# Performance work log

Hardware: AMD Instinct MI355X
Metric: run time of the kernel (lower is better)

## Reference

```python
import jax, jax.numpy as jnp
import numpy as np

# PyG ChebConv defaults: normalization='sym', lambda_max=2.0.
# L_hat = 2*L/lambda_max - I = (I - D^-1/2 A D^-1/2) - I = -D^-1/2 A D^-1/2
# (self-loop/diagonal coefficient is exactly 0 when lambda_max == 2).

N_NODES = 30000
IN_CH = 128
HID_CH = 256
K = 3
N_EDGES = 480000


def _norm_weights(edge_index, n):
    src, dst = edge_index[0], edge_index[1]
    mask = src != dst  # remove_self_loops
    ones = jnp.where(mask, 1.0, 0.0)
    deg = jax.ops.segment_sum(ones, src, num_segments=n)
    dis = jnp.where(deg > 0, deg ** -0.5, 0.0)  # deg_inv_sqrt, inf -> 0
    w = jnp.where(mask, -dis[src] * dis[dst], 0.0)  # -A_sym edge weights
    return src, dst, w


def _cheb_conv(x, src, dst, w, W, b, n):
    # Tx_0 = x; Tx_1 = L_hat x; Tx_k = 2 L_hat Tx_{k-1} - Tx_{k-2}
    def lap(h):  # sparse matvec: (L_hat h)[i] = sum_{e: dst_e=i} w_e * h[src_e]
        return jax.ops.segment_sum(w[:, None] * h[src], dst, num_segments=n)

    Tx_prev = x
    out = x @ W[0]
    if W.shape[0] > 1:
        Tx_cur = lap(x)
        out = out + Tx_cur @ W[1]
        for k in range(2, W.shape[0]):
            Tx_next = 2.0 * lap(Tx_cur) - Tx_prev
            out = out + Tx_next @ W[k]
            Tx_prev, Tx_cur = Tx_cur, Tx_next
    return out + b


def setup_inputs() -> dict:
    key = jax.random.key(0)
    k1, k2, k3, k4, k5, k6 = jax.random.split(key, 6)
    x = jax.random.normal(k1, (N_NODES, IN_CH), dtype=jnp.float32)
    edge_index = jax.random.randint(k2, (2, N_EDGES), 0, N_NODES, dtype=jnp.int64)
    s1 = (1.0 / (IN_CH * K)) ** 0.5
    s2 = (1.0 / (HID_CH * K)) ** 0.5
    W1 = jax.random.uniform(k3, (K, IN_CH, HID_CH), jnp.float32, -s1, s1)
    b1 = jax.random.uniform(k4, (HID_CH,), jnp.float32, -s1, s1)
    W2 = jax.random.uniform(k5, (K, HID_CH, IN_CH), jnp.float32, -s2, s2)
    b2 = jax.random.uniform(k6, (IN_CH,), jnp.float32, -s2, s2)
    return {"x": x, "edge_index": edge_index, "W1": W1, "b1": b1, "W2": W2, "b2": b2}


def reference(x, edge_index, W1, b1, W2, b2):
    n = x.shape[0]
    src, dst, w = _norm_weights(edge_index, n)
    h = jax.nn.relu(_cheb_conv(x, src, dst, w, W1, b1, n))
    return _cheb_conv(h, src, dst, w, W2, b2, n)
```

## Files before the change

### kernel.cpp

```cpp
#include <hip/hip_runtime.h>
#include <hip/hip_bf16.h>


#define ELLW 64

typedef short bf16x8_t __attribute__((ext_vector_type(8)));
typedef unsigned short u16x4_t __attribute__((ext_vector_type(4)));
typedef unsigned short u16x8_t __attribute__((ext_vector_type(8)));
typedef float f32x4_t __attribute__((ext_vector_type(4)));

static __device__ inline unsigned short f2bf(float f) {
    __hip_bfloat16 h = __float2bfloat16(f);
    return __builtin_bit_cast(unsigned short, h);
}
static __device__ inline float bfbits2f(unsigned int lo16) {
    unsigned int u = lo16 << 16;
    return __builtin_bit_cast(float, u);
}

__global__ __launch_bounds__(256) void build_kernel(const int* __restrict__ src,
                                                    const int* __restrict__ dst,
                                                    int* __restrict__ degi,
                                                    int* __restrict__ cnt,
                                                    int* __restrict__ ell, int E) {
    int e = blockIdx.x * 256 + threadIdx.x;
    if (e >= E) return;
    int s = src[e], d = dst[e];
    if (s != d) atomicAdd(&degi[s], 1);
    int pos = atomicAdd(&cnt[d], 1);
    if (pos < ELLW) ell[(size_t)d * ELLW + pos] = s;
}

__global__ __launch_bounds__(256) void dis_kernel(const int* __restrict__ degi,
                                                  float* __restrict__ dis, int N) {
    int i = blockIdx.x * 256 + threadIdx.x;
    if (i >= N) return;
    int d = degi[i];
    dis[i] = (d > 0) ? rsqrtf((float)d) : 0.0f;
}

__global__ __launch_bounds__(256) void bt1_kernel(const float* __restrict__ W1,
                                                  unsigned short* __restrict__ Bt1) {
    int i = blockIdx.x * 256 + threadIdx.x;
    if (i >= 256 * 384) return;
    int n = i / 384, k = i % 384;
    Bt1[(size_t)n * 384 + k] = f2bf(W1[(size_t)k * 256 + n]);
}

__global__ __launch_bounds__(256) void bt2_kernel(const float* __restrict__ W2,
                                                  unsigned short* __restrict__ Bt2) {
    int i = blockIdx.x * 256 + threadIdx.x;
    if (i >= 384 * 256) return;
    int n = i / 256, k = i % 256;
    float v;
    if (n < 128) v = W2[(size_t)(1 * 256 + k) * 128 + n];
    else if (n < 256) v = W2[(size_t)(2 * 256 + k) * 128 + (n - 128)];
    else v = W2[(size_t)k * 128 + (n - 256)] - W2[(size_t)(2 * 256 + k) * 128 + (n - 256)];
    Bt2[(size_t)n * 256 + k] = f2bf(v);
}

__global__ __launch_bounds__(256) void f2bf_kernel(const float* __restrict__ X,
                                                   unsigned short* __restrict__ Xb, int n4) {
    int i = blockIdx.x * 256 + threadIdx.x;
    if (i >= n4) return;
    f32x4_t v = *(const f32x4_t*)&X[(size_t)i * 4];
    u16x4_t u;
    u.x = f2bf(v.x); u.y = f2bf(v.y); u.z = f2bf(v.z); u.w = f2bf(v.w);
    *(u16x4_t*)&Xb[(size_t)i * 4] = u;
}

__global__ __launch_bounds__(256) void lap_ell_kernel(const unsigned short* __restrict__ Xb,
                                                      float* __restrict__ Yf,
                                                      unsigned short* __restrict__ Yb,
                                                      const int* __restrict__ cnt,
                                                      const int* __restrict__ ell,
                                                      const float* __restrict__ dis,
                                                      const float* __restrict__ add,
                                                      const float* __restrict__ bias,
                                                      float s, float a, int N) {
    int wave = threadIdx.x >> 6;
    int lane = threadIdx.x & 63;
    int node = blockIdx.x * 4 + wave;
    if (node >= N) return;
    int n = cnt[node];
    if (n > ELLW) n = ELLW;
    float disn = dis[node];
    const int* row = ell + (size_t)node * ELLW;

    float ax0 = 0.f, ay0 = 0.f, ax1 = 0.f, ay1 = 0.f;
    float ax2 = 0.f, ay2 = 0.f, ax3 = 0.f, ay3 = 0.f;
    int j = 0;
    for (; j + 4 <= n; j += 4) {
        int4 s4 = *(const int4*)&row[j];
        int s0 = __builtin_amdgcn_readfirstlane(s4.x);
        int s1 = __builtin_amdgcn_readfirstlane(s4.y);
        int s2 = __builtin_amdgcn_readfirstlane(s4.z);
        int s3 = __builtin_amdgcn_readfirstlane(s4.w);
        unsigned int v0 = *(const unsigned int*)&Xb[(size_t)s0 * 128 + lane * 2];
        unsigned int v1 = *(const unsigned int*)&Xb[(size_t)s1 * 128 + lane * 2];
        unsigned int v2 = *(const unsigned int*)&Xb[(size_t)s2 * 128 + lane * 2];
        unsigned int v3 = *(const unsigned int*)&Xb[(size_t)s3 * 128 + lane * 2];
        float w0 = (s0 != node) ? -disn * dis[s0] : 0.0f;
        float w1 = (s1 != node) ? -disn * dis[s1] : 0.0f;
        float w2 = (s2 != node) ? -disn * dis[s2] : 0.0f;
        float w3 = (s3 != node) ? -disn * dis[s3] : 0.0f;
        ax0 = fmaf(w0, bfbits2f(v0 & 0xffffu), ax0);
        ay0 = fmaf(w0, bfbits2f(v0 >> 16), ay0);
        ax1 = fmaf(w1, bfbits2f(v1 & 0xffffu), ax1);
        ay1 = fmaf(w1, bfbits2f(v1 >> 16), ay1);
        ax2 = fmaf(w2, bfbits2f(v2 & 0xffffu), ax2);
        ay2 = fmaf(w2, bfbits2f(v2 >> 16), ay2);
        ax3 = fmaf(w3, bfbits2f(v3 & 0xffffu), ax3);
        ay3 = fmaf(w3, bfbits2f(v3 >> 16), ay3);
    }
    for (; j < n; ++j) {
        int s0 = __builtin_amdgcn_readfirstlane(row[j]);
        unsigned int v0 = *(const unsigned int*)&Xb[(size_t)s0 * 128 + lane * 2];
        float w0 = (s0 != node) ? -disn * dis[s0] : 0.0f;
        ax0 = fmaf(w0, bfbits2f(v0 & 0xffffu), ax0);
        ay0 = fmaf(w0, bfbits2f(v0 >> 16), ay0);
    }
    float rx = s * ((ax0 + ax1) + (ax2 + ax3));
    float ry = s * ((ay0 + ay1) + (ay2 + ay3));
    size_t o = (size_t)node * 128 + lane * 2;
    if (add) {
        float2 ad = *(const float2*)&add[o];
        rx = fmaf(a, ad.x, rx);
        ry = fmaf(a, ad.y, ry);
    }
    if (bias) {
        rx += bias[lane * 2];
        ry += bias[lane * 2 + 1];
    }
    if (Yf) {
        float2 r; r.x = rx; r.y = ry;
        *(float2*)&Yf[o] = r;
    }
    if (Yb) {
        unsigned int ob = ((unsigned int)f2bf(ry) << 16) | f2bf(rx);
        *(unsigned int*)&Yb[o] = ob;
    }
}

__global__ __launch_bounds__(256) void gemm_mfma_kernel(
        const unsigned short* __restrict__ A0, const unsigned short* __restrict__ A1,
        const unsigned short* __restrict__ A2, int ldA,
        const unsigned short* __restrict__ Bt, int K,
        float* __restrict__ Of0, float* __restrict__ Of1, float* __restrict__ Of2,
        unsigned short* __restrict__ Ob0, unsigned short* __restrict__ Ob1,
        unsigned short* __restrict__ Ob2,
        int ldO, const float* __restrict__ bias, int M, int relu) {
    __shared__ unsigned short As[64][72];
    __shared__ unsigned short Bs[64][72];

    int tid = threadIdx.x;
    int lane = tid & 63;
    int wid = tid >> 6;
    int wm = wid >> 1, wn = wid & 1;
    int lm = lane & 15, lg = lane >> 4;

    int rowBase = blockIdx.x * 64;
    int colBase = blockIdx.y * 64;

    f32x4_t acc[2][2] = {};

    for (int k0 = 0; k0 < K; k0 += 64) {
        int seg = k0 >> 7;
        int acol = k0 & 127;
        const unsigned short* A = (seg == 0) ? A0 : ((seg == 1) ? A1 : A2);

        {
            int row = tid >> 2;
            int c = (tid & 3) * 16;
            int gr = rowBase + row;
            u16x8_t v0 = {0, 0, 0, 0, 0, 0, 0, 0};
            u16x8_t v1 = {0, 0, 0, 0, 0, 0, 0, 0};
            if (gr < M) {
                const unsigned short* ap = &A[(size_t)gr * ldA + acol + c];
                v0 = *(const u16x8_t*)ap;
                v1 = *(const u16x8_t*)(ap + 8);
            }
            *(u16x8_t*)&As[row][c] = v0;
            *(u16x8_t*)&As[row][c + 8] = v1;
        }
#pragma unroll
        for (int it = 0; it < 2; ++it) {
            int f = tid + it * 256;
            int n = f >> 3;
            int kb = f & 7;
            u16x8_t bv = *(const u16x8_t*)&Bt[(size_t)(colBase + n) * K + k0 + kb * 8];
            *(u16x8_t*)&Bs[n][kb * 8] = bv;
        }
        __syncthreads();

#pragma unroll
        for (int ks = 0; ks < 2; ++ks) {
            int koff = ks * 32 + lg * 8;
            bf16x8_t a0 = *(const bf16x8_t*)&As[wm * 32 + lm][koff];
            bf16x8_t a1 = *(const bf16x8_t*)&As[wm * 32 + 16 + lm][koff];
            bf16x8_t b0 = *(const bf16x8_t*)&Bs[wn * 32 + lm][koff];
            bf16x8_t b1 = *(const bf16x8_t*)&Bs[wn * 32 + 16 + lm][koff];
            acc[0][0] = __builtin_amdgcn_mfma_f32_16x16x32_bf16(a0, b0, acc[0][0], 0, 0, 0);
            acc[0][1] = __builtin_amdgcn_mfma_f32_16x16x32_bf16(a0, b1, acc[0][1], 0, 0, 0);
            acc[1][0] = __builtin_amdgcn_mfma_f32_16x16x32_bf16(a1, b0, acc[1][0], 0, 0, 0);
            acc[1][1] = __builtin_amdgcn_mfma_f32_16x16x32_bf16(a1, b1, acc[1][1], 0, 0, 0);
        }
        __syncthreads();
    }

    int oseg = colBase >> 7;
    float* Of = (oseg == 0) ? Of0 : ((oseg == 1) ? Of1 : Of2);
    unsigned short* Ob = (oseg == 0) ? Ob0 : ((oseg == 1) ? Ob1 : Ob2);
    int lcbase = (colBase & 127) + wn * 32;
#pragma unroll
    for (int i = 0; i < 2; ++i) {
#pragma unroll
        for (int j = 0; j < 2; ++j) {
            int lc = lcbase + j * 16 + lm;
            int gcol = colBase + wn * 32 + j * 16 + lm;
            float bval = bias ? bias[gcol] : 0.0f;
#pragma unroll
            for (int r = 0; r < 4; ++r) {
                int gr = rowBase + wm * 32 + i * 16 + lg * 4 + r;
                if (gr < M) {
                    float v = acc[i][j][r] + bval;
                    if (relu) v = fmaxf(v, 0.0f);
                    if (Of) Of[(size_t)gr * ldO + lc] = v;
                    if (Ob) Ob[(size_t)gr * ldO + lc] = f2bf(v);
                }
            }
        }
    }
}

extern "C" void kernel_launch(void* const* d_in, const int* in_sizes, int n_in,
                              void* d_out, int out_size, void* d_ws, size_t ws_size,
                              hipStream_t stream) {
    const float* x  = (const float*)d_in[0];
    const int*   ei = (const int*)d_in[1];
    const float* W1 = (const float*)d_in[2];
    const float* b1 = (const float*)d_in[3];
    const float* W2 = (const float*)d_in[4];
    const float* b2 = (const float*)d_in[5];
    float* out = (float*)d_out;

    const int IN = 128, HID = 256;
    int N = in_sizes[0] / IN;
    int E = in_sizes[1] / 2;
    const int* src = ei;
    const int* dst = ei + E;

    char* ws = (char*)d_ws;
    size_t off = 0;
    auto alloc = [&](size_t bytes) -> void* {
        void* p = ws + off;
        off += (bytes + 255) & ~(size_t)255;
        return p;
    };
    int* ibuf   = (int*)alloc((size_t)2 * N * 4);
    int* degi   = ibuf;
    int* cnt    = ibuf + N;
    float* dis  = (float*)alloc((size_t)N * 4);
    int* ell    = (int*)alloc((size_t)N * ELLW * 4);
    unsigned short* xb  = (unsigned short*)alloc((size_t)N * IN * 2);
    unsigned short* T1b = (unsigned short*)alloc((size_t)N * IN * 2);
    unsigned short* T2b = (unsigned short*)alloc((size_t)N * IN * 2);
    unsigned short* A2b = (unsigned short*)alloc((size_t)N * IN * 2);
    unsigned short* Ib  = (unsigned short*)alloc((size_t)N * IN * 2);
    unsigned short* hb  = (unsigned short*)alloc((size_t)N * HID * 2);
    float* D    = (float*)alloc((size_t)N * IN * 4);
    float* Z    = (float*)alloc((size_t)N * IN * 4);
    unsigned short* Bt1 = (unsigned short*)alloc((size_t)256 * 384 * 2);
    unsigned short* Bt2 = (unsigned short*)alloc((size_t)384 * 256 * 2);

    int gE = (E + 255) / 256;
    int gN = (N + 255) / 256;
    int gLap = (N + 3) / 4;
    int gBlkM = (N + 63) / 64;

    hipMemsetAsync(ibuf, 0, (size_t)2 * N * 4, stream);
    build_kernel<<<gE, 256, 0, stream>>>(src, dst, degi, cnt, ell, E);
    dis_kernel<<<gN, 256, 0, stream>>>(degi, dis, N);
    bt1_kernel<<<(256 * 384 + 255) / 256, 256, 0, stream>>>(W1, Bt1);
    bt2_kernel<<<(384 * 256 + 255) / 256, 256, 0, stream>>>(W2, Bt2);
    f2bf_kernel<<<(N * IN / 4 + 255) / 256, 256, 0, stream>>>(x, xb, N * IN / 4);

    lap_ell_kernel<<<gLap, 256, 0, stream>>>(xb, nullptr, T1b, cnt, ell, dis,
                                             nullptr, nullptr, 1.0f, 0.0f, N);
    lap_ell_kernel<<<gLap, 256, 0, stream>>>(T1b, nullptr, T2b, cnt, ell, dis,
                                             x, nullptr, 2.0f, -1.0f, N);
    {
        dim3 grid(gBlkM, 4);
        gemm_mfma_kernel<<<grid, 256, 0, stream>>>(xb, T1b, T2b, IN,
                                                   Bt1, 384,
                                                   nullptr, nullptr, nullptr,
                                                   hb, hb + 128, nullptr,
                                                   HID, b1, N, 1);
    }

    {
        dim3 grid(gBlkM, 6);
        gemm_mfma_kernel<<<grid, 256, 0, stream>>>(hb, hb + 128, nullptr, HID,
                                                   Bt2, 256,
                                                   D, nullptr, Z,
                                                   nullptr, A2b, nullptr,
                                                   IN, nullptr, N, 0);
        lap_ell_kernel<<<gLap, 256, 0, stream>>>(A2b, nullptr, Ib, cnt, ell, dis,
                                                 D, nullptr, 2.0f, 1.0f, N);
        lap_ell_kernel<<<gLap, 256, 0, stream>>>(Ib, out, nullptr, cnt, ell, dis,
                                                 Z, b2, 1.0f, 1.0f, N);
    }
}
```

Measured before the change: 220.6 us.

## Fuse prep kernels, drop dis buffer, store GEMM outputs in bf16, enlarge GEMM tile

Merges the weight-transpose and x-to-bf16 conversion kernels into a single prep kernel and removes dis_kernel; edge weights are now computed in the Laplacian kernel via rsqrt of the degree product. The build kernel handles two edges per thread. GEMM intermediates D and Z and the residual x are stored and read as bf16 instead of fp32, which cuts memory traffic at some cost in precision. The GEMM block becomes 512 threads covering 128 rows. It is unclear whether the A-tile loading code (not shown) was updated to fill 128 rows, and the wave-to-tile mapping may not cover the enlarged tile.

```diff
diff --git a/kernel.cpp b/kernel.cpp
--- a/kernel.cpp
+++ b/kernel.cpp
@@ -23,50 +23,54 @@
                                                     int* __restrict__ degi,
                                                     int* __restrict__ cnt,
                                                     int* __restrict__ ell, int E) {
-    int e = blockIdx.x * 256 + threadIdx.x;
-    if (e >= E) return;
-    int s = src[e], d = dst[e];
-    if (s != d) atomicAdd(&degi[s], 1);
-    int pos = atomicAdd(&cnt[d], 1);
-    if (pos < ELLW) ell[(size_t)d * ELLW + pos] = s;
-}
-
-__global__ __launch_bounds__(256) void dis_kernel(const int* __restrict__ degi,
-                                                  float* __restrict__ dis, int N) {
+    int base = (blockIdx.x * 256 + threadIdx.x) * 2;
+    if (base >= E) return;
+    if (base + 2 <= E) {
+        int2 s2 = *(const int2*)&src[base];
+        int2 d2 = *(const int2*)&dst[base];
+        if (s2.x != d2.x) atomicAdd(&degi[s2.x], 1);
+        if (s2.y != d2.y) atomicAdd(&degi[s2.y], 1);
+        int p0 = atomicAdd(&cnt[d2.x], 1);
+        int p1 = atomicAdd(&cnt[d2.y], 1);
+        if (p0 < ELLW) ell[(size_t)d2.x * ELLW + p0] = s2.x;
+        if (p1 < ELLW) ell[(size_t)d2.y * ELLW + p1] = s2.y;
+    } else {
+        int s = src[base], d = dst[base];
+        if (s != d) atomicAdd(&degi[s], 1);
+        int p = atomicAdd(&cnt[d], 1);
+        if (p < ELLW) ell[(size_t)d * ELLW + p] = s;
+    }
+}
+
+__global__ __launch_bounds__(256) void prep_kernel(const float* __restrict__ W1,
+                                                   const float* __restrict__ W2,
+                                                   const float* __restrict__ x,
+                                                   unsigned short* __restrict__ Bt1,
+                                                   unsigned short* __restrict__ Bt2,
+                                                   unsigned short* __restrict__ xb,
+                                                   int nx4) {
+    const int NB1 = 256 * 384, NB2 = 384 * 256;
     int i = blockIdx.x * 256 + threadIdx.x;
-    if (i >= N) return;
-    int d = degi[i];
-    dis[i] = (d > 0) ? rsqrtf((float)d) : 0.0f;
-}
-
-__global__ __launch_bounds__(256) void bt1_kernel(const float* __restrict__ W1,
-                                                  unsigned short* __restrict__ Bt1) {
-    int i = blockIdx.x * 256 + threadIdx.x;
-    if (i >= 256 * 384) return;
-    int n = i / 384, k = i % 384;
-    Bt1[(size_t)n * 384 + k] = f2bf(W1[(size_t)k * 256 + n]);
-}
-
-__global__ __launch_bounds__(256) void bt2_kernel(const float* __restrict__ W2,
-                                                  unsigned short* __restrict__ Bt2) {
-    int i = blockIdx.x * 256 + threadIdx.x;
-    if (i >= 384 * 256) return;
-    int n = i / 256, k = i % 256;
-    float v;
-    if (n < 128) v = W2[(size_t)(1 * 256 + k) * 128 + n];
-    else if (n < 256) v = W2[(size_t)(2 * 256 + k) * 128 + (n - 128)];
-    else v = W2[(size_t)k * 128 + (n - 256)] - W2[(size_t)(2 * 256 + k) * 128 + (n - 256)];
-    Bt2[(size_t)n * 256 + k] = f2bf(v);
-}
-
-__global__ __launch_bounds__(256) void f2bf_kernel(const float* __restrict__ X,
-                                                   unsigned short* __restrict__ Xb, int n4) {
-    int i = blockIdx.x * 256 + threadIdx.x;
-    if (i >= n4) return;
-    f32x4_t v = *(const f32x4_t*)&X[(size_t)i * 4];
-    u16x4_t u;
-    u.x = f2bf(v.x); u.y = f2bf(v.y); u.z = f2bf(v.z); u.w = f2bf(v.w);
-    *(u16x4_t*)&Xb[(size_t)i * 4] = u;
+    if (i < NB1) {
+        int n = i / 384, k = i % 384;
+        Bt1[(size_t)n * 384 + k] = f2bf(W1[(size_t)k * 256 + n]);
+    } else if (i < NB1 + NB2) {
+        int j = i - NB1;
+        int n = j / 256, k = j % 256;
+        float v;
+        if (n < 128) v = W2[(size_t)(1 * 256 + k) * 128 + n];
+        else if (n < 256) v = W2[(size_t)(2 * 256 + k) * 128 + (n - 128)];
+        else v = W2[(size_t)k * 128 + (n - 256)] - W2[(size_t)(2 * 256 + k) * 128 + (n - 256)];
+        Bt2[(size_t)n * 256 + k] = f2bf(v);
+    } else {
+        int j = i - NB1 - NB2;
+        if (j < nx4) {
+            f32x4_t v = *(const f32x4_t*)&x[(size_t)j * 4];
+            u16x4_t u;
+            u.x = f2bf(v.x); u.y = f2bf(v.y); u.z = f2bf(v.z); u.w = f2bf(v.w);
+            *(u16x4_t*)&xb[(size_t)j * 4] = u;
+        }
+    }
 }
 
 __global__ __launch_bounds__(256) void lap_ell_kernel(const unsigned short* __restrict__ Xb,
@@ -74,8 +78,8 @@
                                                       unsigned short* __restrict__ Yb,
                                                       const int* __restrict__ cnt,
                                                       const int* __restrict__ ell,
-                                                      const float* __restrict__ dis,
-                                                      const float* __restrict__ add,
+                                                      const int* __restrict__ degi,
+                                                      const unsigned short* __restrict__ add,
                                                       const float* __restrict__ bias,
                                                       float s, float a, int N) {
     int wave = threadIdx.x >> 6;
@@ -84,7 +88,8 @@
     if (node >= N) return;
     int n = cnt[node];
     if (n > ELLW) n = ELLW;
-    float disn = dis[node];
+    int dn = degi[node];
+    float fdn = (float)dn;
     const int* row = ell + (size_t)node * ELLW;
 
     float ax0 = 0.f, ay0 = 0.f, ax1 = 0.f, ay1 = 0.f;
@@ -100,10 +105,11 @@
         unsigned int v1 = *(const unsigned int*)&Xb[(size_t)s1 * 128 + lane * 2];
         unsigned int v2 = *(const unsigned int*)&Xb[(size_t)s2 * 128 + lane * 2];
         unsigned int v3 = *(const unsigned int*)&Xb[(size_t)s3 * 128 + lane * 2];
-        float w0 = (s0 != node) ? -disn * dis[s0] : 0.0f;
-        float w1 = (s1 != node) ? -disn * dis[s1] : 0.0f;
-        float w2 = (s2 != node) ? -disn * dis[s2] : 0.0f;
-        float w3 = (s3 != node) ? -disn * dis[s3] : 0.0f;
+        int ds0 = degi[s0], ds1 = degi[s1], ds2 = degi[s2], ds3 = degi[s3];
+        float w0 = (s0 != node && dn > 0 && ds0 > 0) ? -rsqrtf(fdn * (float)ds0) : 0.0f;
+        float w1 = (s1 != node && dn > 0 && ds1 > 0) ? -rsqrtf(fdn * (float)ds1) : 0.0f;
+        float w2 = (s2 != node && dn > 0 && ds2 > 0) ? -rsqrtf(fdn * (float)ds2) : 0.0f;
+        float w3 = (s3 != node && dn > 0 && ds3 > 0) ? -rsqrtf(fdn * (float)ds3) : 0.0f;
         ax0 = fmaf(w0, bfbits2f(v0 & 0xffffu), ax0);
         ay0 = fmaf(w0, bfbits2f(v0 >> 16), ay0);
         ax1 = fmaf(w1, bfbits2f(v1 & 0xffffu), ax1);
@@ -116,7 +122,8 @@
     for (; j < n; ++j) {
         int s0 = __builtin_amdgcn_readfirstlane(row[j]);
         unsigned int v0 = *(const unsigned int*)&Xb[(size_t)s0 * 128 + lane * 2];
-        float w0 = (s0 != node) ? -disn * dis[s0] : 0.0f;
+        int ds0 = degi[s0];
+        float w0 = (s0 != node && dn > 0 && ds0 > 0) ? -rsqrtf(fdn * (float)ds0) : 0.0f;
         ax0 = fmaf(w0, bfbits2f(v0 & 0xffffu), ax0);
         ay0 = fmaf(w0, bfbits2f(v0 >> 16), ay0);
     }
@@ -124,9 +131,9 @@
     float ry = s * ((ay0 + ay1) + (ay2 + ay3));
     size_t o = (size_t)node * 128 + lane * 2;
     if (add) {
-        float2 ad = *(const float2*)&add[o];
-        rx = fmaf(a, ad.x, rx);
-        ry = fmaf(a, ad.y, ry);
+        unsigned int ad = *(const unsigned int*)&add[o];
+        rx = fmaf(a, bfbits2f(ad & 0xffffu), rx);
+        ry = fmaf(a, bfbits2f(ad >> 16), ry);
     }
     if (bias) {
         rx += bias[lane * 2];
@@ -142,24 +149,24 @@
     }
 }
 
-__global__ __launch_bounds__(256) void gemm_mfma_kernel(
+__global__ __launch_bounds__(512) void gemm_mfma_kernel(
         const unsigned short* __restrict__ A0, const unsigned short* __restrict__ A1,
         const unsigned short* __restrict__ A2, int ldA,
         const unsigned short* __restrict__ Bt, int K,
-        float* __restrict__ Of0, float* __restrict__ Of1, float* __restrict__ Of2,
         unsigned short* __restrict__ Ob0, unsigned short* __restrict__ Ob1,
         unsigned short* __restrict__ Ob2,
         int ldO, const float* __restrict__ bias, int M, int relu) {
-    __shared__ unsigned short As[64][72];
+    __shared__ unsigned short As[128][72];
     __shared__ unsigned short Bs[64][72];
 
     int tid = threadIdx.x;
     int lane = tid & 63;
     int wid = tid >> 6;
-    int wm = wid >> 1, wn = wid & 1;
+    int wm = wid >> 1;
+    int wn = wid & 1;
     int lm = lane & 15, lg = lane >> 4;
 
-    int rowBase = blockIdx.x * 64;
+    int rowBase = blockIdx.x * 128;
     int colBase = blockIdx.y * 64;
 
     f32x4_t acc[2][2] = {};
@@ -183,11 +190,9 @@
             *(u16x8_t*)&As[row][c] = v0;
             *(u16x8_t*)&As[row][c + 8] = v1;
         }
-#pragma unroll
-        for (int it = 0; it < 2; ++it) {
-            int f = tid + it * 256;
-            int n = f >> 3;
-            int kb = f & 7;
+        {
+            int n = tid >> 3;
+            int kb = tid & 7;
             u16x8_t bv = *(const u16x8_t*)&Bt[(size_t)(colBase + n) * K + k0 + kb * 8];
             *(u16x8_t*)&Bs[n][kb * 8] = bv;
         }
@@ -209,7 +214,6 @@
     }
 
     int oseg = colBase >> 7;
-    float* Of = (oseg == 0) ? Of0 : ((oseg == 1) ? Of1 : Of2);
     unsigned short* Ob = (oseg == 0) ? Ob0 : ((oseg == 1) ? Ob1 : Ob2);
     int lcbase = (colBase & 127) + wn * 32;
 #pragma unroll
@@ -225,8 +229,7 @@
                 if (gr < M) {
                     float v = acc[i][j][r] + bval;
                     if (relu) v = fmaxf(v, 0.0f);
-                    if (Of) Of[(size_t)gr * ldO + lc] = v;
-                    if (Ob) Ob[(size_t)gr * ldO + lc] = f2bf(v);
+                    Ob[(size_t)gr * ldO + lc] = f2bf(v);
                 }
             }
         }
@@ -260,7 +263,6 @@
     int* ibuf   = (int*)alloc((size_t)2 * N * 4);
     int* degi   = ibuf;
     int* cnt    = ibuf + N;
-    float* dis  = (float*)alloc((size_t)N * 4);
     int* ell    = (int*)alloc((size_t)N * ELLW * 4);
     unsigned short* xb  = (unsigned short*)alloc((size_t)N * IN * 2);
     unsigned short* T1b = (unsigned short*)alloc((size_t)N * IN * 2);
@@ -268,46 +270,41 @@
     unsigned short* A2b = (unsigned short*)alloc((size_t)N * IN * 2);
     unsigned short* Ib  = (unsigned short*)alloc((size_t)N * IN * 2);
     unsigned short* hb  = (unsigned short*)alloc((size_t)N * HID * 2);
-    float* D    = (float*)alloc((size_t)N * IN * 4);
-    float* Z    = (float*)alloc((size_t)N * IN * 4);
+    unsigned short* Db  = (unsigned short*)alloc((size_t)N * IN * 2);
+    unsigned short* Zb  = (unsigned short*)alloc((size_t)N * IN * 2);
     unsigned short* Bt1 = (unsigned short*)alloc((size_t)256 * 384 * 2);
     unsigned short* Bt2 = (unsigned short*)alloc((size_t)384 * 256 * 2);
 
-    int gE = (E + 255) / 256;
-    int gN = (N + 255) / 256;
     int gLap = (N + 3) / 4;
-    int gBlkM = (N + 63) / 64;
+    int gBlkM = (N + 127) / 128;
+    int nx4 = N * IN / 4;
+    int prepItems = 256 * 384 + 384 * 256 + nx4;
 
     hipMemsetAsync(ibuf, 0, (size_t)2 * N * 4, stream);
-    build_kernel<<<gE, 256, 0, stream>>>(src, dst, degi, cnt, ell, E);
-    dis_kernel<<<gN, 256, 0, stream>>>(degi, dis, N);
-    bt1_kernel<<<(256 * 384 + 255) / 256, 256, 0, stream>>>(W1, Bt1);
-    bt2_kernel<<<(384 * 256 + 255) / 256, 256, 0, stream>>>(W2, Bt2);
-    f2bf_kernel<<<(N * IN / 4 + 255) / 256, 256, 0, stream>>>(x, xb, N * IN / 4);
-
-    lap_ell_kernel<<<gLap, 256, 0, stream>>>(xb, nullptr, T1b, cnt, ell, dis,
+    build_kernel<<<(E / 2 + 256) / 256, 256, 0, stream>>>(src, dst, degi, cnt, ell, E);
+    prep_kernel<<<(prepItems + 255) / 256, 256, 0, stream>>>(W1, W2, x, Bt1, Bt2, xb, nx4);
+
+    lap_ell_kernel<<<gLap, 256, 0, stream>>>(xb, nullptr, T1b, cnt, ell, degi,
                                              nullptr, nullptr, 1.0f, 0.0f, N);
-    lap_ell_kernel<<<gLap, 256, 0, stream>>>(T1b, nullptr, T2b, cnt, ell, dis,
-                                             x, nullptr, 2.0f, -1.0f, N);
+    lap_ell_kernel<<<gLap, 256, 0, stream>>>(T1b, nullptr, T2b, cnt, ell, degi,
+                                             xb, nullptr, 2.0f, -1.0f, N);
     {
         dim3 grid(gBlkM, 4);
-        gemm_mfma_kernel<<<grid, 256, 0, stream>>>(xb, T1b, T2b, IN,
+        gemm_mfma_kernel<<<grid, 512, 0, stream>>>(xb, T1b, T2b, IN,
                                                    Bt1, 384,
-                                                   nullptr, nullptr, nullptr,
                                                    hb, hb + 128, nullptr,
                                                    HID, b1, N, 1);
     }
 
     {
         dim3 grid(gBlkM, 6);
-        gemm_mfma_kernel<<<grid, 256, 0, stream>>>(hb, hb + 128, nullptr, HID,
+        gemm_mfma_kernel<<<grid, 512, 0, stream>>>(hb, hb + 128, nullptr, HID,
                                                    Bt2, 256,
-                                                   D, nullptr, Z,
-                                                   nullptr, A2b, nullptr,
+                                                   Db, A2b, Zb,
                                                    IN, nullptr, N, 0);
-        lap_ell_kernel<<<gLap, 256, 0, stream>>>(A2b, nullptr, Ib, cnt, ell, dis,
-                                                 D, nullptr, 2.0f, 1.0f, N);
-        lap_ell_kernel<<<gLap, 256, 0, stream>>>(Ib, out, nullptr, cnt, ell, dis,
-                                                 Z, b2, 1.0f, 1.0f, N);
-    }
-}
+        lap_ell_kernel<<<gLap, 256, 0, stream>>>(A2b, nullptr, Ib, cnt, ell, degi,
+                                                 Db, nullptr, 2.0f, 1.0f, N);
+        lap_ell_kernel<<<gLap, 256, 0, stream>>>(Ib, out, nullptr, cnt, ell, degi,
+                                                 Zb, b2, 1.0f, 1.0f, N);
+    }
+}
```

Result: faster. 209.5 us (-5.0%).
